# Kernel tuning notes

Measured on AMD Instinct MI355X. Metric: run time of the kernel, lower is better.

## Reference

```python
import jax, jax.numpy as jnp
import numpy as np

B = 2          # number of point clouds (batch vector has B blocks)
N_PER = 16384  # points per cloud
F = 32         # input feature dim
D = 3          # coordinate dim
RATIO = 0.25
R = 0.2        # ball-query radius
K = 64         # max_neighbors
H1 = 64        # MLP hidden
COUT = 128     # MLP output
M = int(N_PER * RATIO)  # centroids per cloud


def setup_inputs() -> dict:
    key = jax.random.key(0)
    k0, k1, k2, k3 = jax.random.split(key, 4)
    x = jax.random.normal(k0, (B * N_PER, F), jnp.float32)
    pos = jax.random.uniform(k1, (B * N_PER, D), jnp.float32)
    batch = jnp.repeat(jnp.arange(B), N_PER)
    W1 = jax.random.normal(k2, (F + D, H1), jnp.float32) / np.sqrt(F + D)
    b1 = jnp.zeros((H1,), jnp.float32)
    W2 = jax.random.normal(k3, (H1, COUT), jnp.float32) / np.sqrt(H1)
    b2 = jnp.zeros((COUT,), jnp.float32)
    return {"x": x, "pos": pos, "batch": batch, "W1": W1, "b1": b1, "W2": W2, "b2": b2}


def _fps(pos_b):
    """Iterative farthest point sampling: (N_PER, D) -> (M,) indices."""
    d0 = jnp.sum((pos_b - pos_b[0]) ** 2, axis=-1)  # start at point 0

    def body(d, _):
        i = jnp.argmax(d)
        d = jnp.minimum(d, jnp.sum((pos_b - pos_b[i]) ** 2, axis=-1))
        return d, i

    _, idxs = jax.lax.scan(body, d0, None, length=M - 1)
    return jnp.concatenate([jnp.zeros((1,), idxs.dtype), idxs])


def _set_abstraction(x_b, pos_b, W1, b1, W2, b2):
    idx = _fps(pos_b)            # (M,)
    pc = pos_b[idx]              # centroid positions (M, D)
    # ball query: squared distances centroids -> all points, capped at K neighbors
    d2 = jnp.sum((pc[:, None, :] - pos_b[None, :, :]) ** 2, axis=-1)  # (M, N_PER)
    neg = jnp.where(d2 <= R * R, -d2, -jnp.inf)
    vals, nbr = jax.lax.top_k(neg, K)        # K nearest within radius
    valid = vals > -jnp.inf                  # (M, K)
    xj = x_b[nbr]                            # (M, K, F)
    pj = pos_b[nbr]                          # (M, K, D)
    # faithful to source: msg = pos_j - pos_i / r  (note: pos_i/r, not (pos_j-pos_i)/r)
    msg = jnp.concatenate([xj, pj - pc[:, None, :] / R], axis=-1)  # (M, K, F+D)
    h = jax.nn.relu(msg @ W1 + b1) @ W2 + b2                       # (M, K, COUT)
    h = jnp.where(valid[:, :, None], h, -jnp.inf)
    out = jnp.max(h, axis=1)                 # max aggregation over neighbors
    out = jnp.where(jnp.isfinite(out), out, 0.0)
    return out, pc


def reference(x, pos, batch, W1, b1, W2, b2):
    xb = x.reshape(B, N_PER, F)
    pb = pos.reshape(B, N_PER, D)
    out, pc = jax.vmap(lambda xx, pp: _set_abstraction(xx, pp, W1, b1, W2, b2))(xb, pb)
    batch_out = jnp.repeat(jnp.arange(B, dtype=batch.dtype), M)
    return out.reshape(B * M, COUT), pc.reshape(B * M, D), batch_out
```

## Files before the change

### kernel.cpp

```cpp
#include <hip/hip_runtime.h>
#include <hip/hip_bf16.h>

#define NPTS 16384
#define MCENT 4096
#define BCLD 2
#define FDIM 32
#define H1DIM 64
#define CODIM 128
#define KNBR 64
#define R2CUT 0.04f

__device__ __forceinline__ float d2e(float ax, float ay, float az,
                                     float bx, float by, float bz) {
  float dx = __fsub_rn(ax, bx);
  float dy = __fsub_rn(ay, by);
  float dz = __fsub_rn(az, bz);
  return __fadd_rn(__fadd_rn(__fmul_rn(dx, dx), __fmul_rn(dy, dy)), __fmul_rn(dz, dz));
}

__device__ __forceinline__ int spread3(int v) {
  return ((v & 4) << 4) | ((v & 2) << 2) | (v & 1);
}
__device__ __forceinline__ int cell_of(float x, float y, float z) {
  int cx = min(7, (int)(x * 8.0f));
  int cy = min(7, (int)(y * 8.0f));
  int cz = min(7, (int)(z * 8.0f));
  return (spread3(cx) << 2) | (spread3(cy) << 1) | spread3(cz);
}

#define DPP_LEXMAX_STEP(bb, nn, ctrl)                                          \
  do {                                                                         \
    unsigned _ob = (unsigned)__builtin_amdgcn_update_dpp(0, (int)(bb), ctrl,   \
                                                         0xf, 0xf, false);     \
    unsigned _on = (unsigned)__builtin_amdgcn_update_dpp(0, (int)(nn), ctrl,   \
                                                         0xf, 0xf, false);     \
    bool _t = (_ob > (bb)) || (_ob == (bb) && _on > (nn));                     \
    (bb) = _t ? _ob : (bb);                                                    \
    (nn) = _t ? _on : (nn);                                                    \
  } while (0)

__device__ __forceinline__ int rdlane(int v, int l) {
  return __builtin_amdgcn_readlane(v, l);
}
__device__ __forceinline__ float rdlanef(float v, int l) {
  return __int_as_float(__builtin_amdgcn_readlane(__float_as_int(v), l));
}

__global__ __attribute__((amdgpu_flat_work_group_size(1024, 1024),
                          amdgpu_waves_per_eu(4, 4)))
void fps_kernel(const float* __restrict__ pos,
                int* __restrict__ fps_idx,
                float4* __restrict__ ws_sorted) {
  const int b = blockIdx.x;
  const float* P = pos + (size_t)b * NPTS * 3;
  float4* S = ws_sorted + (size_t)b * NPTS;
  const int tid = threadIdx.x;
  const int lane = tid & 63;
  const int wave = tid >> 6;

  __shared__ int hist[512];
  __shared__ int offs[512];
  __shared__ unsigned long long skey[2][16];
  __shared__ float4 spos[2][16];
  __shared__ int winners[MCENT];

  if (tid < 512) hist[tid] = 0;
  __syncthreads();
#pragma unroll 4
  for (int j = 0; j < 16; ++j) {
    int i = tid + j * 1024;
    float x = P[3 * i + 0], y = P[3 * i + 1], z = P[3 * i + 2];
    atomicAdd(&hist[cell_of(x, y, z)], 1);
  }
  __syncthreads();
  if (tid < 64) {
    int base = tid * 8;
    int loc[8];
    int run = 0;
#pragma unroll
    for (int k = 0; k < 8; ++k) { loc[k] = run; run += hist[base + k]; }
    int inc = run;
#pragma unroll
    for (int off = 1; off < 64; off <<= 1) {
      int o = __shfl_up(inc, off);
      if (tid >= off) inc += o;
    }
    int ex = inc - run;
#pragma unroll
    for (int k = 0; k < 8; ++k) offs[base + k] = ex + loc[k];
  }
  __syncthreads();
#pragma unroll 4
  for (int j = 0; j < 16; ++j) {
    int i = tid + j * 1024;
    float x = P[3 * i + 0], y = P[3 * i + 1], z = P[3 * i + 2];
    int p = atomicAdd(&offs[cell_of(x, y, z)], 1);
    S[p] = make_float4(x, y, z, __int_as_float(i));
  }
  __syncthreads();

  float px[16], py[16], pz[16], d[16];
  unsigned nidx[16];
  const float x0 = P[0], y0 = P[1], z0 = P[2];
  float bxm, bxM, bym, byM, bzm, bzM;
  unsigned tb = 0u, tn = 0u;
  float tx = 0.f, ty = 0.f, tz = 0.f;
#pragma unroll
  for (int j = 0; j < 16; ++j) {
    float4 v = S[tid * 16 + j];
    px[j] = v.x; py[j] = v.y; pz[j] = v.z;
    nidx[j] = ~(unsigned)__float_as_int(v.w);
    float dj = d2e(v.x, v.y, v.z, x0, y0, z0);
    d[j] = dj;
    if (j == 0) {
      bxm = v.x; bxM = v.x; bym = v.y; byM = v.y; bzm = v.z; bzM = v.z;
    } else {
      bxm = fminf(bxm, v.x); bxM = fmaxf(bxM, v.x);
      bym = fminf(bym, v.y); byM = fmaxf(byM, v.y);
      bzm = fminf(bzm, v.z); bzM = fmaxf(bzM, v.z);
    }
    unsigned db = __float_as_uint(dj);
    unsigned nj = nidx[j];
    bool t = (db > tb) || (db == tb && nj > tn);
    tb = t ? db : tb; tn = t ? nj : tn;
    tx = t ? v.x : tx; ty = t ? v.y : ty; tz = t ? v.z : tz;
  }

  if (tid == 0) winners[0] = 0;

  bool wavedirty = true;
  unsigned cwb = 0u, cwn = 0u;
  float cwx = 0.f, cwy = 0.f, cwz = 0.f;

  for (int m = 1; m < MCENT; ++m) {
    const int par = m & 1;

    if (wavedirty) {
      unsigned bb = tb, nn = tn;
      DPP_LEXMAX_STEP(bb, nn, 0x111);
      DPP_LEXMAX_STEP(bb, nn, 0x112);
      DPP_LEXMAX_STEP(bb, nn, 0x114);
      DPP_LEXMAX_STEP(bb, nn, 0x118);
      DPP_LEXMAX_STEP(bb, nn, 0x142);
      DPP_LEXMAX_STEP(bb, nn, 0x143);
      cwb = (unsigned)rdlane((int)bb, 63);
      cwn = (unsigned)rdlane((int)nn, 63);
      unsigned long long own = __ballot(tb == cwb && tn == cwn);
      int ol = (int)__ffsll(own) - 1;
      cwx = rdlanef(tx, ol);
      cwy = rdlanef(ty, ol);
      cwz = rdlanef(tz, ol);
    }
    if (lane == 0) {
      skey[par][wave] = ((unsigned long long)cwb << 32) | (unsigned long long)cwn;
      spos[par][wave] = make_float4(cwx, cwy, cwz, 0.0f);
    }
    __syncthreads();

    unsigned rb, rn;
    unsigned sb0 = 0u, sn0 = 0u;
    {
      unsigned bb = 0u, nn = 0u;
      if (lane < 16) {
        unsigned long long kk = skey[par][lane];
        bb = (unsigned)(kk >> 32);
        nn = (unsigned)kk;
        sb0 = bb; sn0 = nn;
        DPP_LEXMAX_STEP(bb, nn, 0x111);
        DPP_LEXMAX_STEP(bb, nn, 0x112);
        DPP_LEXMAX_STEP(bb, nn, 0x114);
        DPP_LEXMAX_STEP(bb, nn, 0x118);
      }
      rb = (unsigned)rdlane((int)bb, 15);
      rn = (unsigned)rdlane((int)nn, 15);
    }
    unsigned long long wm = __ballot(lane < 16 && sb0 == rb && sn0 == rn);
    int ws = (int)__ffsll(wm) - 1;
    float4 wp = spos[par][ws];
    if (tid == 0) winners[m] = (int)(~rn);

    float ex = fmaxf(fmaxf(bxm - wp.x, wp.x - bxM), 0.0f);
    float ey = fmaxf(fmaxf(bym - wp.y, wp.y - byM), 0.0f);
    float ez = fmaxf(fmaxf(bzm - wp.z, wp.z - bzM), 0.0f);
    float lb = (ex * ex + ey * ey + ez * ez) * 0.999f;
    bool mydirty = lb < __uint_as_float(tb);
    if (mydirty) {
      unsigned nb = 0u, nn2 = 0u;
      float nx = 0.f, ny = 0.f, nz = 0.f;
#pragma unroll
      for (int j = 0; j < 16; ++j) {
        float dj = fminf(d[j], d2e(px[j], py[j], pz[j], wp.x, wp.y, wp.z));
        d[j] = dj;
        unsigned db = __float_as_uint(dj);
        unsigned nj = nidx[j];
        bool t = (db > nb) || (db == nb && nj > nn2);
        nb = t ? db : nb; nn2 = t ? nj : nn2;
        nx = t ? px[j] : nx; ny = t ? py[j] : ny; nz = t ? pz[j] : nz;
      }
      tb = nb; tn = nn2; tx = nx; ty = ny; tz = nz;
    }
    wavedirty = (__ballot(mydirty) != 0ULL);
  }

  __syncthreads();
  for (int i = tid; i < MCENT; i += 1024) fps_idx[b * MCENT + i] = winners[i];
}

__global__ __launch_bounds__(256) void ballq_kernel(const float* __restrict__ pos,
                                                    const int* __restrict__ fps_idx,
                                                    int* __restrict__ nbr,
                                                    float* __restrict__ out_pc,
                                                    float* __restrict__ out_batch) {
  const int wave = threadIdx.x >> 6;
  const int lane = threadIdx.x & 63;
  const int c = blockIdx.x * 4 + wave;
  const int b = c >> 12;
  const float* P = pos + (size_t)b * NPTS * 3;

  const int ci = fps_idx[c];
  const float cx = P[3 * ci + 0];
  const float cy = P[3 * ci + 1];
  const float cz = P[3 * ci + 2];
  if (lane == 0) {
    out_pc[3 * c + 0] = cx;
    out_pc[3 * c + 1] = cy;
    out_pc[3 * c + 2] = cz;
    out_batch[c] = (float)b;
  }

  __shared__ unsigned long long list[4][1024];
  __shared__ int cnt[4];
  if (lane == 0) cnt[wave] = 0;

  for (int i = lane; i < NPTS; i += 64) {
    const float qx = P[3 * i + 0];
    const float qy = P[3 * i + 1];
    const float qz = P[3 * i + 2];
    const float dd = d2e(cx, cy, cz, qx, qy, qz);
    if (dd <= R2CUT) {
      int p = atomicAdd(&cnt[wave], 1);
      if (p < 1024)
        list[wave][p] = ((unsigned long long)__float_as_uint(dd) << 32)
                      | (unsigned long long)(unsigned)i;
    }
  }
  __syncthreads();

  int n = cnt[wave];
  if (n > 1024) n = 1024;

  unsigned long long loc[16];
#pragma unroll
  for (int k = 0; k < 16; ++k) {
    int i = lane + k * 64;
    loc[k] = (i < n) ? list[wave][i] : ~0ULL;
  }
  unsigned long long mv = loc[0];
#pragma unroll
  for (int k = 1; k < 16; ++k)
    if (loc[k] < mv) mv = loc[k];

  int myout = -1;
  for (int s = 0; s < 64; ++s) {
    unsigned long long wmin = mv;
#pragma unroll
    for (int off = 32; off >= 1; off >>= 1) {
      unsigned long long o = __shfl_xor(wmin, off);
      if (o < wmin) wmin = o;
    }
    if (lane == s) myout = (wmin == ~0ULL) ? -1 : (int)(unsigned)wmin;
    if (mv == wmin && wmin != ~0ULL) {
#pragma unroll
      for (int k = 0; k < 16; ++k)
        if (loc[k] == wmin) loc[k] = ~0ULL;
      mv = loc[0];
#pragma unroll
      for (int k = 1; k < 16; ++k)
        if (loc[k] < mv) mv = loc[k];
    }
  }
  nbr[c * KNBR + lane] = myout;
}

__global__ __launch_bounds__(256) void mlp_kernel(const float* __restrict__ pos,
                                                  const float* __restrict__ x,
                                                  const int* __restrict__ fps_idx,
                                                  const int* __restrict__ nbr,
                                                  const float* __restrict__ W1,
                                                  const float* __restrict__ b1,
                                                  const float* __restrict__ W2,
                                                  const float* __restrict__ b2,
                                                  float* __restrict__ out) {
  const int c = blockIdx.x;
  const int b = c >> 12;
  const float* P = pos + (size_t)b * NPTS * 3;
  const float* X = x + (size_t)b * NPTS * FDIM;

  __shared__ float W1s[35 * 64];
  __shared__ float W2s[64 * 128];
  __shared__ float b1s[64];
  __shared__ float b2s[128];
  __shared__ float h1s[64][64];
  __shared__ float pmax[2][128];
  __shared__ int validk[64];

  const int tid = threadIdx.x;
  for (int i = tid; i < 35 * 64; i += 256) W1s[i] = W1[i];
  for (int i = tid; i < 64 * 128; i += 256) W2s[i] = W2[i];
  if (tid < 64) b1s[tid] = b1[tid];
  else if (tid < 192) b2s[tid - 64] = b2[tid - 64];

  const int ci = fps_idx[c];
  const float c5x = P[3 * ci + 0] / 0.2f;
  const float c5y = P[3 * ci + 1] / 0.2f;
  const float c5z = P[3 * ci + 2] / 0.2f;

  const int k = tid >> 2, q = tid & 3;
  const int nk = nbr[c * KNBR + k];
  if (q == 0) validk[k] = (nk >= 0) ? 1 : 0;
  const int nkc = (nk < 0) ? 0 : nk;

  float msg[35];
  const float4* Xr = (const float4*)(X + (size_t)nkc * FDIM);
#pragma unroll
  for (int i4 = 0; i4 < 8; ++i4) {
    float4 v = Xr[i4];
    msg[i4 * 4 + 0] = v.x; msg[i4 * 4 + 1] = v.y;
    msg[i4 * 4 + 2] = v.z; msg[i4 * 4 + 3] = v.w;
  }
  msg[32] = P[3 * nkc + 0] - c5x;
  msg[33] = P[3 * nkc + 1] - c5y;
  msg[34] = P[3 * nkc + 2] - c5z;

  __syncthreads();

  float acc[16];
#pragma unroll
  for (int h = 0; h < 16; ++h) acc[h] = b1s[q * 16 + h];
#pragma unroll
  for (int i = 0; i < 35; ++i) {
    const float m = msg[i];
    const float4* wrow = (const float4*)&W1s[i * 64 + q * 16];
#pragma unroll
    for (int j4 = 0; j4 < 4; ++j4) {
      float4 w = wrow[j4];
      acc[j4 * 4 + 0] += m * w.x;
      acc[j4 * 4 + 1] += m * w.y;
      acc[j4 * 4 + 2] += m * w.z;
      acc[j4 * 4 + 3] += m * w.w;
    }
  }
#pragma unroll
  for (int h = 0; h < 16; ++h) h1s[k][q * 16 + h] = fmaxf(acc[h], 0.0f);
  __syncthreads();

  const int ch = tid & 127, half = tid >> 7;
  float w2r[64];
#pragma unroll
  for (int i = 0; i < 64; ++i) w2r[i] = W2s[i * 128 + ch];

  float mx = -INFINITY;
  for (int k2 = half * 32; k2 < half * 32 + 32; ++k2) {
    if (!validk[k2]) continue;
    float s = b2s[ch];
    const float4* hr = (const float4*)h1s[k2];
#pragma unroll
    for (int i4 = 0; i4 < 16; ++i4) {
      float4 h4 = hr[i4];
      s += h4.x * w2r[i4 * 4 + 0] + h4.y * w2r[i4 * 4 + 1]
         + h4.z * w2r[i4 * 4 + 2] + h4.w * w2r[i4 * 4 + 3];
    }
    mx = fmaxf(mx, s);
  }
  pmax[half][ch] = mx;
  __syncthreads();

  if (tid < 128) {
    float m2 = fmaxf(pmax[0][tid], pmax[1][tid]);
    out[(size_t)c * CODIM + tid] = (m2 > -INFINITY) ? m2 : 0.0f;
  }
}

extern "C" void kernel_launch(void* const* d_in, const int* in_sizes, int n_in,
                              void* d_out, int out_size, void* d_ws, size_t ws_size,
                              hipStream_t stream) {
  const float* x   = (const float*)d_in[0];
  const float* pos = (const float*)d_in[1];
  const float* W1  = (const float*)d_in[3];
  const float* b1  = (const float*)d_in[4];
  const float* W2  = (const float*)d_in[5];
  const float* b2  = (const float*)d_in[6];
  float* out = (float*)d_out;

  int* fps_idx = (int*)d_ws;
  int* nbr     = (int*)d_ws + BCLD * MCENT;
  float4* ws_sorted = (float4*)nbr;

  float* out_pc    = out + (size_t)BCLD * MCENT * CODIM;
  float* out_batch = out_pc + (size_t)BCLD * MCENT * 3;

  hipLaunchKernelGGL(fps_kernel, dim3(BCLD), dim3(1024), 0, stream, pos, fps_idx, ws_sorted);
  hipLaunchKernelGGL(ballq_kernel, dim3(BCLD * MCENT / 4), dim3(256), 0, stream,
                     pos, fps_idx, nbr, out_pc, out_batch);
  hipLaunchKernelGGL(mlp_kernel, dim3(BCLD * MCENT), dim3(256), 0, stream,
                     pos, x, fps_idx, nbr, W1, b1, W2, b2, out);
}
```

Baseline: 7.800 ms.

## Stream FPS point data from global memory each iteration instead of holding it in registers

The farthest-point-sampling loop no longer keeps each thread's 16 points (x, y, z and index) in registers. Instead it reloads them every iteration with inline-asm global_load_dwordx4 instructions issued ahead of the wave and block reductions, so the loads overlap that work. The block barrier becomes a raw s_barrier that waits only on LDS traffic, which lets the global loads stay in flight across it. This is meant to cut register pressure for the 1024-thread block, at the cost of about 256 bytes of L2/cache traffic per thread on each of the ~4K iterations, plus hand-managed waitcnt ordering.

After: 28.97 ms. 3.71x slower.

```diff
diff --git a/kernel.cpp b/kernel.cpp
--- a/kernel.cpp
+++ b/kernel.cpp
@@ -9,6 +9,8 @@
 #define CODIM 128
 #define KNBR 64
 #define R2CUT 0.04f
+
+typedef float f32x4 __attribute__((ext_vector_type(4)));
 
 __device__ __forceinline__ float d2e(float ax, float ay, float az,
                                      float bx, float by, float bz) {
@@ -99,8 +101,7 @@
   }
   __syncthreads();
 
-  float px[16], py[16], pz[16], d[16];
-  unsigned nidx[16];
+  float d[16];
   const float x0 = P[0], y0 = P[1], z0 = P[2];
   float bxm, bxM, bym, byM, bzm, bzM;
   unsigned tb = 0u, tn = 0u;
@@ -108,8 +109,6 @@
 #pragma unroll
   for (int j = 0; j < 16; ++j) {
     float4 v = S[tid * 16 + j];
-    px[j] = v.x; py[j] = v.y; pz[j] = v.z;
-    nidx[j] = ~(unsigned)__float_as_int(v.w);
     float dj = d2e(v.x, v.y, v.z, x0, y0, z0);
     d[j] = dj;
     if (j == 0) {
@@ -120,20 +119,49 @@
       bzm = fminf(bzm, v.z); bzM = fmaxf(bzM, v.z);
     }
     unsigned db = __float_as_uint(dj);
-    unsigned nj = nidx[j];
+    unsigned nj = ~(unsigned)__float_as_int(v.w);
     bool t = (db > tb) || (db == tb && nj > tn);
     tb = t ? db : tb; tn = t ? nj : tn;
     tx = t ? v.x : tx; ty = t ? v.y : ty; tz = t ? v.z : tz;
   }
 
   if (tid == 0) winners[0] = 0;
+  __syncthreads();
 
   bool wavedirty = true;
   unsigned cwb = 0u, cwn = 0u;
   float cwx = 0.f, cwy = 0.f, cwz = 0.f;
 
+  const unsigned voff = (unsigned)tid * 256u;
+  const float4* Sp = S;
+
   for (int m = 1; m < MCENT; ++m) {
     const int par = m & 1;
+
+    f32x4 r0, r1, r2, r3, r4, r5, r6, r7, r8, r9, r10, r11, r12, r13, r14, r15;
+    asm volatile("s_waitcnt vmcnt(0)" ::: "memory");
+    asm volatile(
+        "global_load_dwordx4 %0, %16, %17 offset:0\n\t"
+        "global_load_dwordx4 %1, %16, %17 offset:16\n\t"
+        "global_load_dwordx4 %2, %16, %17 offset:32\n\t"
+        "global_load_dwordx4 %3, %16, %17 offset:48\n\t"
+        "global_load_dwordx4 %4, %16, %17 offset:64\n\t"
+        "global_load_dwordx4 %5, %16, %17 offset:80\n\t"
+        "global_load_dwordx4 %6, %16, %17 offset:96\n\t"
+        "global_load_dwordx4 %7, %16, %17 offset:112\n\t"
+        "global_load_dwordx4 %8, %16, %17 offset:128\n\t"
+        "global_load_dwordx4 %9, %16, %17 offset:144\n\t"
+        "global_load_dwordx4 %10, %16, %17 offset:160\n\t"
+        "global_load_dwordx4 %11, %16, %17 offset:176\n\t"
+        "global_load_dwordx4 %12, %16, %17 offset:192\n\t"
+        "global_load_dwordx4 %13, %16, %17 offset:208\n\t"
+        "global_load_dwordx4 %14, %16, %17 offset:224\n\t"
+        "global_load_dwordx4 %15, %16, %17 offset:240"
+        : "=v"(r0), "=v"(r1), "=v"(r2), "=v"(r3),
+          "=v"(r4), "=v"(r5), "=v"(r6), "=v"(r7),
+          "=v"(r8), "=v"(r9), "=v"(r10), "=v"(r11),
+          "=v"(r12), "=v"(r13), "=v"(r14), "=v"(r15)
+        : "v"(voff), "s"(Sp));
 
     if (wavedirty) {
       unsigned bb = tb, nn = tn;
@@ -155,7 +183,10 @@
       skey[par][wave] = ((unsigned long long)cwb << 32) | (unsigned long long)cwn;
       spos[par][wave] = make_float4(cwx, cwy, cwz, 0.0f);
     }
-    __syncthreads();
+    __builtin_amdgcn_sched_barrier(0);
+    asm volatile("s_waitcnt lgkmcnt(0)" ::: "memory");
+    __builtin_amdgcn_s_barrier();
+    __builtin_amdgcn_sched_barrier(0);
 
     unsigned rb, rn;
     unsigned sb0 = 0u, sn0 = 0u;
@@ -185,18 +216,25 @@
     float lb = (ex * ex + ey * ey + ez * ez) * 0.999f;
     bool mydirty = lb < __uint_as_float(tb);
     if (mydirty) {
+      asm volatile("s_waitcnt vmcnt(0)" ::: "memory");
+      __builtin_amdgcn_sched_barrier(0);
       unsigned nb = 0u, nn2 = 0u;
       float nx = 0.f, ny = 0.f, nz = 0.f;
-#pragma unroll
-      for (int j = 0; j < 16; ++j) {
-        float dj = fminf(d[j], d2e(px[j], py[j], pz[j], wp.x, wp.y, wp.z));
-        d[j] = dj;
-        unsigned db = __float_as_uint(dj);
-        unsigned nj = nidx[j];
-        bool t = (db > nb) || (db == nb && nj > nn2);
-        nb = t ? db : nb; nn2 = t ? nj : nn2;
-        nx = t ? px[j] : nx; ny = t ? py[j] : ny; nz = t ? pz[j] : nz;
+#define UPD(j, rr)                                                             \
+      {                                                                        \
+        float dj = fminf(d[j], d2e((rr).x, (rr).y, (rr).z, wp.x, wp.y, wp.z)); \
+        d[j] = dj;                                                             \
+        unsigned db = __float_as_uint(dj);                                     \
+        unsigned nj = ~(unsigned)__float_as_int((rr).w);                       \
+        bool t = (db > nb) || (db == nb && nj > nn2);                          \
+        nb = t ? db : nb; nn2 = t ? nj : nn2;                                  \
+        nx = t ? (rr).x : nx; ny = t ? (rr).y : ny; nz = t ? (rr).z : nz;      \
       }
+      UPD(0, r0)  UPD(1, r1)  UPD(2, r2)  UPD(3, r3)
+      UPD(4, r4)  UPD(5, r5)  UPD(6, r6)  UPD(7, r7)
+      UPD(8, r8)  UPD(9, r9)  UPD(10, r10) UPD(11, r11)
+      UPD(12, r12) UPD(13, r13) UPD(14, r14) UPD(15, r15)
+#undef UPD
       tb = nb; tn = nn2; tx = nx; ty = ny; tz = nz;
     }
     wavedirty = (__ballot(mydirty) != 0ULL);
```
